# Kernel optimization log

Hardware: AMD Instinct MI355X
Metric: run time of the kernel (lower is better)

Reference implementation:

```python
import jax, jax.numpy as jnp
import numpy as np

B, S, D = 8, 2048, 512

def setup_inputs() -> dict:
    key = jax.random.key(0)
    ks = jax.random.split(key, 9)
    scale = 1.0 / np.sqrt(D)
    q = jax.random.normal(ks[0], (B, S, D), dtype=jnp.float32)
    k = jax.random.normal(ks[1], (B, S, D), dtype=jnp.float32)
    v = jax.random.normal(ks[2], (B, S, D), dtype=jnp.float32)
    # causal mask, broadcast over batch: True = attend
    mask = jnp.tril(jnp.ones((S, S), dtype=bool))[None, :, :]
    Wq = jax.random.normal(ks[3], (D, D), dtype=jnp.float32) * scale
    bq = jax.random.normal(ks[4], (D,), dtype=jnp.float32) * scale
    Wk = jax.random.normal(ks[5], (D, D), dtype=jnp.float32) * scale
    bk = jax.random.normal(ks[6], (D,), dtype=jnp.float32) * scale
    Wv = jax.random.normal(ks[7], (D, D), dtype=jnp.float32) * scale
    bv = jax.random.normal(ks[8], (D,), dtype=jnp.float32) * scale
    return {"q": q, "k": k, "v": v, "mask": mask,
            "Wq": Wq, "bq": bq, "Wk": Wk, "bk": bk, "Wv": Wv, "bv": bv}

def reference(q, k, v, mask, Wq, bq, Wk, bk, Wv, bv):
    # torch nn.Linear: x @ W^T + b
    Q = jnp.einsum('bsd,ed->bse', q, Wq) + bq
    K = jnp.einsum('bsd,ed->bse', k, Wk) + bk
    V = jnp.einsum('bsd,ed->bse', v, Wv) + bv
    scores = jnp.einsum('bqd,bkd->bqk', Q, K) / jnp.sqrt(jnp.float32(D))
    scores = jnp.where(mask, scores, jnp.float32(-1e9))
    prob = jax.nn.softmax(scores, axis=-1)
    out = jnp.einsum('bqk,bkd->bqd', prob, V)
    return out
```

## Files before the change

### kernel.cpp

```cpp
#include <hip/hip_runtime.h>
#include <stdint.h>
#include <stddef.h>
#include <math.h>

typedef _Float16 half8 __attribute__((ext_vector_type(8)));
typedef float f32x4 __attribute__((ext_vector_type(4)));

#define SCALE_QK 0.04419417382415922f

__device__ __forceinline__ void gload16(const void* g, void* lds) {
  __builtin_amdgcn_global_load_lds(
      (const __attribute__((address_space(1))) void*)g,
      (__attribute__((address_space(3))) void*)lds,
      16, 0, 0);
}

__device__ __forceinline__ void run_kloop_wide(const float* Arow0, const _Float16* Brow0,
                                               int lda, int ldb, int kIters,
                                               _Float16* As, _Float16* Bs,
                                               f32x4 (&acc)[4][8])
{
  const int tid  = threadIdx.x;
  const int lane = tid & 63;
  const int w    = tid >> 6;
  const int wm   = w >> 1, wn = w & 1;
  const int srow = tid >> 3;
  const int sg   = tid & 7;
  const int swz  = sg ^ (srow & 7);
  const int fr   = lane & 15;
  const int fq   = lane >> 4;
  const int fx   = lane & 7;

  for (int it = 0; it < kIters; ++it) {
    const int k0 = it * 64;
    f32x4 preF[8];
    #pragma unroll
    for (int i = 0; i < 4; ++i) {
      const float* src = Arow0 + (size_t)(i*32 + srow) * lda + (k0 + sg*8);
      preF[2*i]   = *(const f32x4*)src;
      preF[2*i+1] = *(const f32x4*)(src + 4);
    }
    #pragma unroll
    for (int i = 0; i < 8; ++i)
      gload16(Brow0 + (size_t)(i*32 + srow) * ldb + (k0 + swz*8), Bs + i*2048 + w*512);
    #pragma unroll
    for (int i = 0; i < 4; ++i) {
      f32x4 x = preF[2*i], y = preF[2*i+1];
      half8 h;
      h[0]=(_Float16)x[0]; h[1]=(_Float16)x[1]; h[2]=(_Float16)x[2]; h[3]=(_Float16)x[3];
      h[4]=(_Float16)y[0]; h[5]=(_Float16)y[1]; h[6]=(_Float16)y[2]; h[7]=(_Float16)y[3];
      *(half8*)(As + (i*32 + srow)*64 + swz*8) = h;
    }
    __syncthreads();

    #pragma unroll
    for (int ks = 0; ks < 2; ++ks) {
      half8 av[4], bv[8];
      const int slot = (ks*4 + fq) ^ fx;
      #pragma unroll
      for (int i = 0; i < 4; ++i)
        av[i] = *(const half8*)(As + (wm*64 + i*16 + fr)*64 + slot*8);
      #pragma unroll
      for (int j = 0; j < 8; ++j)
        bv[j] = *(const half8*)(Bs + (wn*128 + j*16 + fr)*64 + slot*8);
      #pragma unroll
      for (int i = 0; i < 4; ++i) {
        #pragma unroll
        for (int j = 0; j < 8; ++j)
          acc[i][j] = __builtin_amdgcn_mfma_f32_16x16x32_f16(av[i], bv[j], acc[i][j], 0, 0, 0);
      }
    }
    __syncthreads();
  }
}

__device__ __forceinline__ void run_kloop_sb(const _Float16* Arow0, const _Float16* Brow0,
                                             int lda, int ldb, int kIters,
                                             _Float16* As, _Float16* Bs,
                                             f32x4 (&acc)[4][4])
{
  const int tid  = threadIdx.x;
  const int lane = tid & 63;
  const int w    = tid >> 6;
  const int wm   = w >> 1, wn = w & 1;
  const int srow = tid >> 3;
  const int sg   = tid & 7;
  const int swz  = sg ^ (srow & 7);
  const int fr   = lane & 15;
  const int fq   = lane >> 4;
  const int fx   = lane & 7;

  for (int it = 0; it < kIters; ++it) {
    const int k0 = it * 64;
    #pragma unroll
    for (int i = 0; i < 4; ++i)
      gload16(Arow0 + (size_t)(i*32 + srow) * lda + (k0 + swz*8), As + i*2048 + w*512);
    #pragma unroll
    for (int i = 0; i < 4; ++i)
      gload16(Brow0 + (size_t)(i*32 + srow) * ldb + (k0 + swz*8), Bs + i*2048 + w*512);
    __syncthreads();

    #pragma unroll
    for (int ks = 0; ks < 2; ++ks) {
      half8 av[4], bv[4];
      const int slot = (ks*4 + fq) ^ fx;
      #pragma unroll
      for (int i = 0; i < 4; ++i) {
        av[i] = *(const half8*)(As + (wm*64 + i*16 + fr)*64 + slot*8);
        bv[i] = *(const half8*)(Bs + (wn*64 + i*16 + fr)*64 + slot*8);
      }
      #pragma unroll
      for (int i = 0; i < 4; ++i) {
        #pragma unroll
        for (int j = 0; j < 4; ++j)
          acc[i][j] = __builtin_amdgcn_mfma_f32_16x16x32_f16(av[i], bv[j], acc[i][j], 0, 0, 0);
      }
    }
    __syncthreads();
  }
}

__global__ __launch_bounds__(256) void k_cvtw(const float* __restrict__ Wq,
                                              const float* __restrict__ Wk,
                                              const float* __restrict__ Wv,
                                              _Float16* __restrict__ Wb)
{
  const int t = blockIdx.x * 256 + threadIdx.x;
  const int base = t * 8;
  const int z = base >> 18;
  const int off = base & 262143;
  const float* src = (z == 0) ? Wq : ((z == 1) ? Wk : Wv);
  f32x4 a = *(const f32x4*)(src + off);
  f32x4 b = *(const f32x4*)(src + off + 4);
  half8 h;
  h[0]=(_Float16)a[0]; h[1]=(_Float16)a[1]; h[2]=(_Float16)a[2]; h[3]=(_Float16)a[3];
  h[4]=(_Float16)b[0]; h[5]=(_Float16)b[1]; h[6]=(_Float16)b[2]; h[7]=(_Float16)b[3];
  *(half8*)(Wb + base) = h;
}

__global__ __launch_bounds__(256, 2) void k_proj(const float* __restrict__ q,
                                                 const float* __restrict__ k,
                                                 const float* __restrict__ v,
                                                 const _Float16* __restrict__ Wb,
                                                 const float* __restrict__ bq,
                                                 const float* __restrict__ bk,
                                                 const float* __restrict__ bv,
                                                 _Float16* __restrict__ Qb,
                                                 _Float16* __restrict__ Kb,
                                                 _Float16* __restrict__ Vt)
{
  __shared__ __align__(16) _Float16 LDSbuf[256*132];
  _Float16* As = LDSbuf;
  _Float16* Bs = LDSbuf + 8192;

  const int bid = blockIdx.x;
  const int xcd = bid & 7, i = bid >> 3;
  const int p = xcd * 48 + (i >> 1);
  const int nt2 = i & 1;
  const int z = p >> 7, mt = p & 127;

  const float* A     = (z == 0) ? q  : (z == 1) ? k  : v;
  const float* bia   = (z == 0) ? bq : (z == 1) ? bk : bv;
  const _Float16* B  = Wb + (size_t)z * 512 * 512;

  f32x4 acc[4][8] = {};
  run_kloop_wide(A + (size_t)mt*128*512, B + (size_t)nt2*256*512, 512, 512, 8,
                 As, Bs, acc);

  const int tid = threadIdx.x;
  const int lane = tid & 63, w = tid >> 6;
  const int wm = w >> 1, wn = w & 1;
  const int fr = lane & 15, fq = lane >> 4;

  if (z < 2) {
    _Float16* C = (z == 0) ? Qb : Kb;
    const float osc = (z == 0) ? SCALE_QK : 1.0f;
    #pragma unroll
    for (int j = 0; j < 8; ++j) {
      const int col = nt2*256 + wn*128 + j*16 + fr;
      const float bval = bia[col];
      #pragma unroll
      for (int i2 = 0; i2 < 4; ++i2) {
        const int row = mt*128 + wm*64 + i2*16 + fq*4;
        #pragma unroll
        for (int r = 0; r < 4; ++r)
          C[(size_t)(row + r) * 512 + col] = (_Float16)((acc[i2][j][r] + bval) * osc);
      }
    }
  } else {
    _Float16* sm = LDSbuf;
    #pragma unroll
    for (int j = 0; j < 8; ++j) {
      const int colloc = wn*128 + j*16 + fr;
      const float bval = bia[nt2*256 + colloc];
      #pragma unroll
      for (int i2 = 0; i2 < 4; ++i2) {
        const int rowloc = wm*64 + i2*16 + fq*4;
        #pragma unroll
        for (int r = 0; r < 4; ++r)
          sm[colloc*132 + rowloc + r] = (_Float16)(acc[i2][j][r] + bval);
      }
    }
    __syncthreads();
    const int bb = mt >> 4, s0 = (mt & 15) * 128;
    #pragma unroll
    for (int q8 = 0; q8 < 16; ++q8) {
      const int dloc = q8*16 + (tid >> 4);
      const int ch   = tid & 15;
      half8 o = *(const half8*)&sm[dloc*132 + ch*8];
      *(half8*)(Vt + ((size_t)bb*512 + nt2*256 + dloc)*2048 + s0 + ch*8) = o;
    }
  }
}

__global__ __launch_bounds__(256, 4) void k_scores(const _Float16* __restrict__ Qb,
                                                   const _Float16* __restrict__ Kb,
                                                   _Float16* __restrict__ P)
{
  __shared__ __align__(16) _Float16 As[128*64], Bs[128*64];
  const int bid = blockIdx.x;
  const int b = bid & 7;
  const int t = bid >> 3;
  int qt = (int)((sqrtf(8.0f * (float)t + 1.0f) - 1.0f) * 0.5f);
  int base = (qt * (qt + 1)) >> 1;
  if (t < base)                { --qt; base = (qt * (qt + 1)) >> 1; }
  else if (t >= base + qt + 1) { ++qt; base = (qt * (qt + 1)) >> 1; }
  const int kt = t - base;

  f32x4 acc[4][4] = {};
  run_kloop_sb(Qb + ((size_t)b*2048 + qt*128)*512,
               Kb + ((size_t)b*2048 + kt*128)*512,
               512, 512, 8, As, Bs, acc);
  const int lane = threadIdx.x & 63, w = threadIdx.x >> 6;
  const int wm = w >> 1, wn = w & 1;
  const int fr = lane & 15, fq = lane >> 4;
  #pragma unroll
  for (int i = 0; i < 4; ++i) {
    const int row = qt*128 + wm*64 + i*16 + fq*4;
    #pragma unroll
    for (int j = 0; j < 4; ++j) {
      const int col = kt*128 + wn*64 + j*16 + fr;
      #pragma unroll
      for (int r = 0; r < 4; ++r)
        P[((size_t)b*2048 + row + r) * 2048 + col] = (_Float16)acc[i][j][r];
    }
  }
}

__global__ __launch_bounds__(256) void k_softmax(_Float16* __restrict__ P)
{
  const int lane = threadIdx.x & 63;
  const int row  = blockIdx.x * 4 + (threadIdx.x >> 6);
  const int qIdx = row & 2047;
  _Float16* p = P + (size_t)row * 2048;
  const int L    = qIdx + 1;
  const int Lpad = ((qIdx >> 7) + 1) * 128;

  half8 xb[4];
  float m = -1e30f, s = 0.f;
  #pragma unroll
  for (int c = 0; c < 4; ++c) {
    const int i0 = lane * 8 + c * 512;
    if (i0 < Lpad) {
      half8 x = *(const half8*)(p + i0);
      xb[c] = x;
      float xv[8];
      #pragma unroll
      for (int j = 0; j < 8; ++j) xv[j] = (i0 + j < L) ? (float)x[j] : -1e30f;
      float cm = xv[0];
      #pragma unroll
      for (int j = 1; j < 8; ++j) cm = fmaxf(cm, xv[j]);
      const float mn = fmaxf(m, cm);
      float cs = 0.f;
      #pragma unroll
      for (int j = 0; j < 8; ++j) cs += __expf(xv[j] - mn);
      s = s * __expf(m - mn) + cs;
      m = mn;
    }
  }
  #pragma unroll
  for (int d = 1; d < 64; d <<= 1) {
    const float mo = __shfl_xor(m, d, 64);
    const float so = __shfl_xor(s, d, 64);
    const float mn = fmaxf(m, mo);
    s = s * __expf(m - mn) + so * __expf(mo - mn);
    m = mn;
  }
  const float inv = 1.0f / s;

  #pragma unroll
  for (int c = 0; c < 4; ++c) {
    const int i0 = lane * 8 + c * 512;
    if (i0 < Lpad) {
      half8 x = xb[c];
      half8 o;
      #pragma unroll
      for (int j = 0; j < 8; ++j)
        o[j] = (i0 + j < L) ? (_Float16)(__expf((float)x[j] - m) * inv) : (_Float16)0.f;
      *(half8*)(p + i0) = o;
    }
  }
}

__global__ __launch_bounds__(256, 4) void k_pv(const _Float16* __restrict__ P,
                                               const _Float16* __restrict__ Vt,
                                               float* __restrict__ Out)
{
  __shared__ __align__(16) _Float16 As[128*64], Bs[128*64];
  const int bid = blockIdx.x;
  const int b = bid & 7;
  const int r0 = bid >> 3;
  const int qi = r0 >> 2, dt = r0 & 3;
  const int qt = (qi & 1) ? (15 - (qi >> 1)) : (qi >> 1);

  f32x4 acc[4][4] = {};
  run_kloop_sb(P  + ((size_t)b*2048 + qt*128)*2048,
               Vt + ((size_t)b*512  + dt*128)*2048,
               2048, 2048, (qt + 1) * 2, As, Bs, acc);
  const int lane = threadIdx.x & 63, w = threadIdx.x >> 6;
  const int wm = w >> 1, wn = w & 1;
  const int fr = lane & 15, fq = lane >> 4;
  #pragma unroll
  for (int i = 0; i < 4; ++i) {
    const int row = qt*128 + wm*64 + i*16 + fq*4;
    #pragma unroll
    for (int j = 0; j < 4; ++j) {
      const int col = dt*128 + wn*64 + j*16 + fr;
      #pragma unroll
      for (int r = 0; r < 4; ++r)
        Out[((size_t)b*2048 + row + r) * 512 + col] = acc[i][j][r];
    }
  }
}

extern "C" void kernel_launch(void* const* d_in, const int* in_sizes, int n_in,
                              void* d_out, int out_size, void* d_ws, size_t ws_size,
                              hipStream_t stream) {
  (void)in_sizes; (void)n_in; (void)out_size;
  const float* q  = (const float*)d_in[0];
  const float* k  = (const float*)d_in[1];
  const float* v  = (const float*)d_in[2];
  const float* Wq = (const float*)d_in[4];
  const float* bq = (const float*)d_in[5];
  const float* Wk = (const float*)d_in[6];
  const float* bk = (const float*)d_in[7];
  const float* Wv = (const float*)d_in[8];
  const float* bv = (const float*)d_in[9];

  const size_t OFF_P  = 0;
  const size_t OFF_Q  = (size_t)64 << 20;
  const size_t OFF_K  = (size_t)80 << 20;
  const size_t OFF_VT = (size_t)112 << 20;
  const size_t OFF_W  = (size_t)128 << 20;
  const size_t NEEDED = OFF_W + (size_t)3 * 512 * 512 * sizeof(_Float16);
  if (ws_size < NEEDED) return;

  char* ws = (char*)d_ws;
  _Float16* P  = (_Float16*)(ws + OFF_P);
  _Float16* Qb = (_Float16*)(ws + OFF_Q);
  _Float16* Kb = (_Float16*)(ws + OFF_K);
  _Float16* Vt = (_Float16*)(ws + OFF_VT);
  _Float16* Wb = (_Float16*)(ws + OFF_W);
  float* Out = (float*)d_out;

  k_cvtw   <<<dim3(384),  dim3(256), 0, stream>>>(Wq, Wk, Wv, Wb);
  k_proj   <<<dim3(768),  dim3(256), 0, stream>>>(q, k, v, Wb, bq, bk, bv, Qb, Kb, Vt);
  k_scores <<<dim3(1088), dim3(256), 0, stream>>>(Qb, Kb, P);
  k_softmax<<<dim3(4096), dim3(256), 0, stream>>>(P);
  k_pv     <<<dim3(512),  dim3(256), 0, stream>>>(P, Vt, Out);
}
```

Before: 266.8 us.

## Load MFMA operands directly from global memory, drop LDS staging in scores and PV

Removes the shared-memory staging loop from the scores and PV GEMMs. Each lane now loads its half8 MFMA fragments straight from global memory, relying on L1/L2 for reuse across waves instead of LDS. This eliminates the __syncthreads barriers and the LDS traffic. The PV kernel is also retiled from 128-wide to 64-wide output column tiles, doubling the grid to 1024 blocks for more parallelism. The cost is redundant global/L2 loads across waves that share rows, and fewer independent MFMAs per load in PV.

New measurement: 416.6 us. 56.2% more time.

```diff
diff --git a/kernel.cpp b/kernel.cpp
--- a/kernel.cpp
+++ b/kernel.cpp
@@ -67,52 +67,6 @@
       for (int i = 0; i < 4; ++i) {
         #pragma unroll
         for (int j = 0; j < 8; ++j)
-          acc[i][j] = __builtin_amdgcn_mfma_f32_16x16x32_f16(av[i], bv[j], acc[i][j], 0, 0, 0);
-      }
-    }
-    __syncthreads();
-  }
-}
-
-__device__ __forceinline__ void run_kloop_sb(const _Float16* Arow0, const _Float16* Brow0,
-                                             int lda, int ldb, int kIters,
-                                             _Float16* As, _Float16* Bs,
-                                             f32x4 (&acc)[4][4])
-{
-  const int tid  = threadIdx.x;
-  const int lane = tid & 63;
-  const int w    = tid >> 6;
-  const int wm   = w >> 1, wn = w & 1;
-  const int srow = tid >> 3;
-  const int sg   = tid & 7;
-  const int swz  = sg ^ (srow & 7);
-  const int fr   = lane & 15;
-  const int fq   = lane >> 4;
-  const int fx   = lane & 7;
-
-  for (int it = 0; it < kIters; ++it) {
-    const int k0 = it * 64;
-    #pragma unroll
-    for (int i = 0; i < 4; ++i)
-      gload16(Arow0 + (size_t)(i*32 + srow) * lda + (k0 + swz*8), As + i*2048 + w*512);
-    #pragma unroll
-    for (int i = 0; i < 4; ++i)
-      gload16(Brow0 + (size_t)(i*32 + srow) * ldb + (k0 + swz*8), Bs + i*2048 + w*512);
-    __syncthreads();
-
-    #pragma unroll
-    for (int ks = 0; ks < 2; ++ks) {
-      half8 av[4], bv[4];
-      const int slot = (ks*4 + fq) ^ fx;
-      #pragma unroll
-      for (int i = 0; i < 4; ++i) {
-        av[i] = *(const half8*)(As + (wm*64 + i*16 + fr)*64 + slot*8);
-        bv[i] = *(const half8*)(Bs + (wn*64 + i*16 + fr)*64 + slot*8);
-      }
-      #pragma unroll
-      for (int i = 0; i < 4; ++i) {
-        #pragma unroll
-        for (int j = 0; j < 4; ++j)
           acc[i][j] = __builtin_amdgcn_mfma_f32_16x16x32_f16(av[i], bv[j], acc[i][j], 0, 0, 0);
       }
     }
@@ -217,7 +171,6 @@
                                                    const _Float16* __restrict__ Kb,
                                                    _Float16* __restrict__ P)
 {
-  __shared__ __align__(16) _Float16 As[128*64], Bs[128*64];
   const int bid = blockIdx.x;
   const int b = bid & 7;
   const int t = bid >> 3;
@@ -227,13 +180,41 @@
   else if (t >= base + qt + 1) { ++qt; base = (qt * (qt + 1)) >> 1; }
   const int kt = t - base;
 
-  f32x4 acc[4][4] = {};
-  run_kloop_sb(Qb + ((size_t)b*2048 + qt*128)*512,
-               Kb + ((size_t)b*2048 + kt*128)*512,
-               512, 512, 8, As, Bs, acc);
   const int lane = threadIdx.x & 63, w = threadIdx.x >> 6;
   const int wm = w >> 1, wn = w & 1;
   const int fr = lane & 15, fq = lane >> 4;
+
+  const _Float16* Aq = Qb + ((size_t)b*2048 + qt*128)*512;
+  const _Float16* Bk = Kb + ((size_t)b*2048 + kt*128)*512;
+  const _Float16* arow[4];
+  const _Float16* brow[4];
+  #pragma unroll
+  for (int i = 0; i < 4; ++i) {
+    arow[i] = Aq + (size_t)(wm*64 + i*16 + fr)*512 + fq*8;
+    brow[i] = Bk + (size_t)(wn*64 + i*16 + fr)*512 + fq*8;
+  }
+
+  f32x4 acc[4][4] = {};
+  #pragma unroll 2
+  for (int it = 0; it < 8; ++it) {
+    const int k0 = it * 64;
+    #pragma unroll
+    for (int ks = 0; ks < 2; ++ks) {
+      half8 av[4], bv[4];
+      #pragma unroll
+      for (int i = 0; i < 4; ++i) {
+        av[i] = *(const half8*)(arow[i] + k0 + ks*32);
+        bv[i] = *(const half8*)(brow[i] + k0 + ks*32);
+      }
+      #pragma unroll
+      for (int i = 0; i < 4; ++i) {
+        #pragma unroll
+        for (int j = 0; j < 4; ++j)
+          acc[i][j] = __builtin_amdgcn_mfma_f32_16x16x32_f16(av[i], bv[j], acc[i][j], 0, 0, 0);
+      }
+    }
+  }
+
   #pragma unroll
   for (int i = 0; i < 4; ++i) {
     const int row = qt*128 + wm*64 + i*16 + fq*4;
@@ -306,26 +287,56 @@
                                                const _Float16* __restrict__ Vt,
                                                float* __restrict__ Out)
 {
-  __shared__ __align__(16) _Float16 As[128*64], Bs[128*64];
   const int bid = blockIdx.x;
   const int b = bid & 7;
   const int r0 = bid >> 3;
-  const int qi = r0 >> 2, dt = r0 & 3;
+  const int qi = r0 >> 3, dt = r0 & 7;
   const int qt = (qi & 1) ? (15 - (qi >> 1)) : (qi >> 1);
-
-  f32x4 acc[4][4] = {};
-  run_kloop_sb(P  + ((size_t)b*2048 + qt*128)*2048,
-               Vt + ((size_t)b*512  + dt*128)*2048,
-               2048, 2048, (qt + 1) * 2, As, Bs, acc);
+  const int kIters = (qt + 1) * 2;
+
   const int lane = threadIdx.x & 63, w = threadIdx.x >> 6;
   const int wm = w >> 1, wn = w & 1;
   const int fr = lane & 15, fq = lane >> 4;
+
+  const _Float16* Ap = P  + ((size_t)b*2048 + qt*128)*2048;
+  const _Float16* Bv = Vt + ((size_t)b*512  + dt*64)*2048;
+  const _Float16* arow[4];
+  const _Float16* brow[2];
+  #pragma unroll
+  for (int i = 0; i < 4; ++i)
+    arow[i] = Ap + (size_t)(wm*64 + i*16 + fr)*2048 + fq*8;
+  #pragma unroll
+  for (int j = 0; j < 2; ++j)
+    brow[j] = Bv + (size_t)(wn*32 + j*16 + fr)*2048 + fq*8;
+
+  f32x4 acc[4][2] = {};
+  #pragma unroll 2
+  for (int it = 0; it < kIters; ++it) {
+    const int k0 = it * 64;
+    #pragma unroll
+    for (int ks = 0; ks < 2; ++ks) {
+      half8 av[4], bv[2];
+      #pragma unroll
+      for (int i = 0; i < 4; ++i)
+        av[i] = *(const half8*)(arow[i] + k0 + ks*32);
+      #pragma unroll
+      for (int j = 0; j < 2; ++j)
+        bv[j] = *(const half8*)(brow[j] + k0 + ks*32);
+      #pragma unroll
+      for (int i = 0; i < 4; ++i) {
+        #pragma unroll
+        for (int j = 0; j < 2; ++j)
+          acc[i][j] = __builtin_amdgcn_mfma_f32_16x16x32_f16(av[i], bv[j], acc[i][j], 0, 0, 0);
+      }
+    }
+  }
+
   #pragma unroll
   for (int i = 0; i < 4; ++i) {
     const int row = qt*128 + wm*64 + i*16 + fq*4;
     #pragma unroll
-    for (int j = 0; j < 4; ++j) {
-      const int col = dt*128 + wn*64 + j*16 + fr;
+    for (int j = 0; j < 2; ++j) {
+      const int col = dt*64 + wn*32 + j*16 + fr;
       #pragma unroll
       for (int r = 0; r < 4; ++r)
         Out[((size_t)b*2048 + row + r) * 512 + col] = acc[i][j][r];
@@ -367,5 +378,5 @@
   k_proj   <<<dim3(768),  dim3(256), 0, stream>>>(q, k, v, Wb, bq, bk, bv, Qb, Kb, Vt);
   k_scores <<<dim3(1088), dim3(256), 0, stream>>>(Qb, Kb, P);
   k_softmax<<<dim3(4096), dim3(256), 0, stream>>>(P);
-  k_pv     <<<dim3(512),  dim3(256), 0, stream>>>(P, Vt, Out);
-}
+  k_pv     <<<dim3(1024), dim3(256), 0, stream>>>(P, Vt, Out);
+}
```

## Tile causal scores kernel as 256x128 blocks pairing two query tiles

Applied to the files above, without the earlier changes.

The QK^T scores kernel now uses 512-thread blocks, each computing a 256x128 tile that covers two adjacent query tiles against one key tile. This lets each K tile loaded into shared memory be reused by both query tiles. Blocks are dispatched with the longest query pairs first, and diagonal tiles write a large negative value above the diagonal. The main loop is written inline with no double buffering, and some computed upper-triangle tiles are thrown away.

Measured after the change: 266.3 us. Within noise of the previous version (-0.2%).

```diff
diff --git a/kernel.cpp b/kernel.cpp
--- a/kernel.cpp
+++ b/kernel.cpp
@@ -213,36 +213,80 @@
   }
 }
 
-__global__ __launch_bounds__(256, 4) void k_scores(const _Float16* __restrict__ Qb,
+__global__ __launch_bounds__(512, 4) void k_scores(const _Float16* __restrict__ Qb,
                                                    const _Float16* __restrict__ Kb,
                                                    _Float16* __restrict__ P)
 {
-  __shared__ __align__(16) _Float16 As[128*64], Bs[128*64];
+  __shared__ __align__(16) _Float16 As[256*64], Bs[128*64];
   const int bid = blockIdx.x;
   const int b = bid & 7;
-  const int t = bid >> 3;
-  int qt = (int)((sqrtf(8.0f * (float)t + 1.0f) - 1.0f) * 0.5f);
-  int base = (qt * (qt + 1)) >> 1;
-  if (t < base)                { --qt; base = (qt * (qt + 1)) >> 1; }
-  else if (t >= base + qt + 1) { ++qt; base = (qt * (qt + 1)) >> 1; }
-  const int kt = t - base;
+  const int t = 71 - (bid >> 3);
+  int qp = 0, accum = 0;
+  while (accum + 2*qp + 2 <= t) { accum += 2*qp + 2; ++qp; }
+  const int kt = t - accum;
+  const int qt0 = 2 * qp;
+
+  const int tid  = threadIdx.x;
+  const int lane = tid & 63;
+  const int w    = tid >> 6;
+  const int wm   = w >> 1, wn = w & 1;
+  const int srow = tid >> 3;
+  const int sg   = tid & 7;
+  const int swz  = sg ^ (srow & 7);
+  const int fr   = lane & 15;
+  const int fq   = lane >> 4;
+  const int fx   = lane & 7;
+
+  const _Float16* Aq = Qb + ((size_t)b*2048 + (size_t)qt0*128)*512;
+  const _Float16* Bk = Kb + ((size_t)b*2048 + (size_t)kt*128)*512;
 
   f32x4 acc[4][4] = {};
-  run_kloop_sb(Qb + ((size_t)b*2048 + qt*128)*512,
-               Kb + ((size_t)b*2048 + kt*128)*512,
-               512, 512, 8, As, Bs, acc);
-  const int lane = threadIdx.x & 63, w = threadIdx.x >> 6;
-  const int wm = w >> 1, wn = w & 1;
-  const int fr = lane & 15, fq = lane >> 4;
-  #pragma unroll
-  for (int i = 0; i < 4; ++i) {
-    const int row = qt*128 + wm*64 + i*16 + fq*4;
-    #pragma unroll
-    for (int j = 0; j < 4; ++j) {
-      const int col = kt*128 + wn*64 + j*16 + fr;
-      #pragma unroll
-      for (int r = 0; r < 4; ++r)
-        P[((size_t)b*2048 + row + r) * 2048 + col] = (_Float16)acc[i][j][r];
+  for (int it = 0; it < 8; ++it) {
+    const int k0 = it * 64;
+    #pragma unroll
+    for (int i = 0; i < 4; ++i)
+      gload16(Aq + (size_t)(i*64 + srow) * 512 + (k0 + swz*8), As + i*4096 + w*512);
+    #pragma unroll
+    for (int i = 0; i < 2; ++i)
+      gload16(Bk + (size_t)(i*64 + srow) * 512 + (k0 + swz*8), Bs + i*4096 + w*512);
+    __syncthreads();
+
+    #pragma unroll
+    for (int ks = 0; ks < 2; ++ks) {
+      half8 av[4], bv[4];
+      const int slot = (ks*4 + fq) ^ fx;
+      #pragma unroll
+      for (int i = 0; i < 4; ++i) {
+        av[i] = *(const half8*)(As + (wm*64 + i*16 + fr)*64 + slot*8);
+        bv[i] = *(const half8*)(Bs + (wn*64 + i*16 + fr)*64 + slot*8);
+      }
+      #pragma unroll
+      for (int i = 0; i < 4; ++i) {
+        #pragma unroll
+        for (int j = 0; j < 4; ++j)
+          acc[i][j] = __builtin_amdgcn_mfma_f32_16x16x32_f16(av[i], bv[j], acc[i][j], 0, 0, 0);
+      }
+    }
+    __syncthreads();
+  }
+
+  const int qt = qt0 + (wm >> 1);
+  if (kt <= qt) {
+    const bool diag = (kt == qt);
+    #pragma unroll
+    for (int i = 0; i < 4; ++i) {
+      const int rl = (wm & 1)*64 + i*16 + fq*4;
+      #pragma unroll
+      for (int j = 0; j < 4; ++j) {
+        const int cl = wn*64 + j*16 + fr;
+        #pragma unroll
+        for (int r = 0; r < 4; ++r) {
+          const float sc = acc[i][j][r];
+          const bool msk = diag && (cl > rl + r);
+          P[((size_t)b*2048 + (size_t)qt*128 + rl + r) * 2048 + kt*128 + cl] =
+              msk ? (_Float16)(-30000.0f) : (_Float16)sc;
+        }
+      }
     }
   }
 }
@@ -365,7 +409,7 @@
 
   k_cvtw   <<<dim3(384),  dim3(256), 0, stream>>>(Wq, Wk, Wv, Wb);
   k_proj   <<<dim3(768),  dim3(256), 0, stream>>>(q, k, v, Wb, bq, bk, bv, Qb, Kb, Vt);
-  k_scores <<<dim3(1088), dim3(256), 0, stream>>>(Qb, Kb, P);
+  k_scores <<<dim3(576),  dim3(512), 0, stream>>>(Qb, Kb, P);
   k_softmax<<<dim3(4096), dim3(256), 0, stream>>>(P);
   k_pv     <<<dim3(512),  dim3(256), 0, stream>>>(P, Vt, Out);
 }
```
